# Performance work log

Measured on AMD Instinct MI355X. Metric: run time of the kernel, lower is better.

Reference implementation:

```python
import jax, jax.numpy as jnp
import numpy as np

GROUP_SIZE = 128
IN_FEATURES = 8192
OUT_FEATURES = 28672
TOKENS = 32


def _dequantize(qweight, qzeros, scales):
    """ExLlama q4 dequant.
    qweight: (K//8, N) int32, 8 int4 values per word packed along k.
    qzeros:  (G, N//8) int32, 8 int4 zeros per word packed along n.
    scales:  (G, N) fp16.  g = k // GROUP_SIZE; w = s * (q - (z + 1)).
    """
    shifts = jnp.arange(8, dtype=jnp.int32) * 4
    K = qweight.shape[0] * 8
    N = qweight.shape[1]
    G = qzeros.shape[0]
    # unpack weights along k: (K//8, 8, N) -> (K, N)
    q = (qweight[:, None, :] >> shifts[None, :, None]) & 15
    q = q.reshape(K, N)
    # unpack zeros along n: (G, N//8, 8) -> (G, N)
    z = (qzeros[:, :, None] >> shifts[None, None, :]) & 15
    z = z.reshape(G, N)
    # group-wise dequant: reshape k into (G, GROUP_SIZE)
    qg = q.reshape(G, GROUP_SIZE, N).astype(jnp.float16)
    zf = (z + 1).astype(jnp.float16)[:, None, :]          # ExLlama stores zero-1
    w = (qg - zf) * scales[:, None, :]                    # (G, GS, N) fp16
    return w.reshape(K, N)


def setup_inputs() -> dict:
    key = jax.random.key(0)
    k1, k2, k3, k4, k5 = jax.random.split(key, 5)
    x = jax.random.normal(k1, (TOKENS, IN_FEATURES), dtype=jnp.float16)
    qweight = jax.random.randint(k2, (IN_FEATURES // 8, OUT_FEATURES),
                                 minval=-(2**31), maxval=2**31 - 1, dtype=jnp.int32)
    qzeros = jax.random.randint(k3, (IN_FEATURES // GROUP_SIZE, OUT_FEATURES // 8),
                                minval=-(2**31), maxval=2**31 - 1, dtype=jnp.int32)
    scales = (jax.random.uniform(k4, (IN_FEATURES // GROUP_SIZE, OUT_FEATURES),
                                 dtype=jnp.float32) * 0.01 + 0.001).astype(jnp.float16)
    bias = jax.random.normal(k5, (OUT_FEATURES,), dtype=jnp.float16)
    return {"x": x, "qweight": qweight, "qzeros": qzeros,
            "scales": scales, "bias": bias}


def reference(x, qweight, qzeros, scales, bias):
    w = _dequantize(qweight, qzeros, scales)              # (K, N) fp16
    out = jnp.matmul(x.astype(jnp.float16), w)            # (T, N)
    return out + bias
```

## Files before the change

kernel.cpp:

```cpp
#include <hip/hip_runtime.h>

#define T_TOK   32
#define KDIM    8192
#define NDIM    28672
#define NZW     3584
#define PHK     256
#define NPH     (KDIM / PHK)
#define GPP     (PHK / 128)
#define XROW    (PHK + 8)
#define XIT     ((T_TOK * PHK) / (256 * 8))

typedef _Float16 half8  __attribute__((ext_vector_type(8)));
typedef _Float16 half2v __attribute__((ext_vector_type(2)));
typedef float    f32x4  __attribute__((ext_vector_type(4)));
typedef unsigned uint4v __attribute__((ext_vector_type(4)));

__global__ __launch_bounds__(256)
void exllama_gemm_fullk(const int*   __restrict__ qweight,
                        const int*   __restrict__ qzeros,
                        const float* __restrict__ scales,
                        const float* __restrict__ x,
                        const float* __restrict__ bias,
                        float*       __restrict__ out)
{
    __shared__ alignas(16) _Float16 xs[2][T_TOK * XROW];

    const int tid  = threadIdx.x;
    const int lane = tid & 63;
    const int wav  = tid >> 6;
    const int quad = lane >> 4;
    const int l16  = lane & 15;
    const int n    = blockIdx.x * 64 + wav * 16 + l16;

    const float* xbase[XIT];
    int          lofs[XIT];
    #pragma unroll
    for (int it = 0; it < XIT; ++it) {
        const int e  = it * 2048 + tid * 8;
        const int t  = e >> 8;
        const int kl = e & (PHK - 1);
        xbase[it] = x + (size_t)t * KDIM + kl;
        lofs[it]  = t * XROW + kl;
    }

    f32x4 xlo[XIT], xhi[XIT];
    auto LOADX = [&](int p) {
        #pragma unroll
        for (int it = 0; it < XIT; ++it) {
            const float* xp = xbase[it] + p * PHK;
            xlo[it] = *(const f32x4*)xp;
            xhi[it] = *(const f32x4*)(xp + 4);
        }
    };
    auto CVTW = [&](_Float16* buf) {
        #pragma unroll
        for (int it = 0; it < XIT; ++it) {
            uint4v u;
            #pragma unroll
            for (int j = 0; j < 4; ++j)
                u[j] = __builtin_bit_cast(unsigned,
                          __builtin_amdgcn_cvt_pkrtz(xlo[it][j], xhi[it][j]));
            *(uint4v*)(buf + lofs[it]) = u;
        }
    };
    auto LOADQ = [&](unsigned* qw, half2v* sp, half2v* cp, int p) {
        #pragma unroll
        for (int g = 0; g < GPP; ++g) {
            const size_t rb = (size_t)(p * (PHK / 8) + g * 16 + quad) * NDIM + n;
            #pragma unroll
            for (int c = 0; c < 4; ++c)
                qw[g * 4 + c] = (unsigned)qweight[rb + (size_t)(c * 4) * NDIM];
            const float s  = scales[(size_t)(p * GPP + g) * NDIM + n];
            const int   zw = qzeros[(size_t)(p * GPP + g) * NZW + (n >> 3)];
            const int   z  = (zw >> ((n & 7) * 4)) & 15;
            const _Float16 sh = (_Float16)s;
            const _Float16 ch = (_Float16)(float)(-(1025 + z));
            sp[g] = (half2v){sh, sh};
            cp[g] = (half2v){ch, ch};
        }
    };

    f32x4 acc0 = (f32x4){0.f, 0.f, 0.f, 0.f};
    f32x4 acc1 = (f32x4){0.f, 0.f, 0.f, 0.f};
    auto COMPUTE = [&](const unsigned* qw, const half2v* sp, const half2v* cp,
                       const _Float16* buf) {
        #pragma unroll
        for (int g = 0; g < GPP; ++g) {
            #pragma unroll
            for (int c = 0; c < 4; ++c) {
                const int kloc = g * 128 + c * 32 + quad * 8;
                half8 a0 = *(const half8*)(buf + l16 * XROW + kloc);
                half8 a1 = *(const half8*)(buf + (l16 + 16) * XROW + kloc);
                const unsigned w = qw[g * 4 + c];
                uint4v bu;
                #pragma unroll
                for (int i = 0; i < 4; ++i) {
                    unsigned t = ((w >> (4 * i)) & 0x000F000Fu) | 0x64006400u;
                    half2v th = __builtin_bit_cast(half2v, t);
                    half2v r  = (th + cp[g]) * sp[g];
                    bu[i] = __builtin_bit_cast(unsigned, r);
                }
                half8 bf = __builtin_bit_cast(half8, bu);
                acc0 = __builtin_amdgcn_mfma_f32_16x16x32_f16(a0, bf, acc0, 0, 0, 0);
                acc1 = __builtin_amdgcn_mfma_f32_16x16x32_f16(a1, bf, acc1, 0, 0, 0);
            }
        }
    };

    unsigned qwA[4 * GPP], qwB[4 * GPP];
    half2v   spA[GPP], cpA[GPP], spB[GPP], cpB[GPP];

    LOADX(0);
    LOADQ(qwA, spA, cpA, 0);
    CVTW(xs[0]);
    __syncthreads();

    for (int pp = 0; pp < NPH; pp += 2) {
        LOADX(pp + 1);
        LOADQ(qwB, spB, cpB, pp + 1);
        COMPUTE(qwA, spA, cpA, xs[0]);
        CVTW(xs[1]);
        __syncthreads();
        if (pp + 2 < NPH) {
            LOADX(pp + 2);
            LOADQ(qwA, spA, cpA, pp + 2);
        }
        COMPUTE(qwB, spB, cpB, xs[1]);
        if (pp + 2 < NPH) CVTW(xs[0]);
        __syncthreads();
    }

    const float bb = bias[n];
    #pragma unroll
    for (int r = 0; r < 4; ++r) {
        out[(size_t)(quad * 4 + r) * NDIM + n]        = acc0[r] + bb;
        out[(size_t)(16 + quad * 4 + r) * NDIM + n]   = acc1[r] + bb;
    }
}

extern "C" void kernel_launch(void* const* d_in, const int* in_sizes, int n_in,
                              void* d_out, int out_size, void* d_ws, size_t ws_size,
                              hipStream_t stream)
{
    const float* x  = (const float*)d_in[0];
    const int* qweight = (const int*)d_in[1];
    const int* qzeros  = (const int*)d_in[2];
    const float* sc = (const float*)d_in[3];
    const float* bs = (const float*)d_in[4];
    float* out      = (float*)d_out;

    (void)d_ws; (void)ws_size;
    exllama_gemm_fullk<<<dim3(NDIM / 64), 256, 0, stream>>>(
        qweight, qzeros, sc, x, bs, out);
}
```

Baseline: 211.0 us.

## Split K across blocks with workspace partials and separate reduce-bias kernel

```diff
diff --git a/kernel.cpp b/kernel.cpp
--- a/kernel.cpp
+++ b/kernel.cpp
@@ -5,24 +5,29 @@
 #define NDIM    28672
 #define NZW     3584
 #define PHK     256
-#define NPH     (KDIM / PHK)
 #define GPP     (PHK / 128)
 #define XROW    (PHK + 8)
 #define XIT     ((T_TOK * PHK) / (256 * 8))
+#define KSPLIT  4
 
 typedef _Float16 half8  __attribute__((ext_vector_type(8)));
 typedef _Float16 half2v __attribute__((ext_vector_type(2)));
 typedef float    f32x4  __attribute__((ext_vector_type(4)));
 typedef unsigned uint4v __attribute__((ext_vector_type(4)));
 
+template<int SPLIT>
 __global__ __launch_bounds__(256)
-void exllama_gemm_fullk(const int*   __restrict__ qweight,
-                        const int*   __restrict__ qzeros,
-                        const float* __restrict__ scales,
-                        const float* __restrict__ x,
-                        const float* __restrict__ bias,
-                        float*       __restrict__ out)
+void exllama_gemm(const int*   __restrict__ qweight,
+                  const int*   __restrict__ qzeros,
+                  const float* __restrict__ scales,
+                  const float* __restrict__ x,
+                  const float* __restrict__ bias,
+                  float*       __restrict__ ws,
+                  float*       __restrict__ out)
 {
+    constexpr int KSEG = KDIM / SPLIT;
+    constexpr int NPH  = KSEG / PHK;
+
     __shared__ alignas(16) _Float16 xs[2][T_TOK * XROW];
 
     const int tid  = threadIdx.x;
@@ -31,6 +36,8 @@
     const int quad = lane >> 4;
     const int l16  = lane & 15;
     const int n    = blockIdx.x * 64 + wav * 16 + l16;
+    const int seg  = (SPLIT > 1) ? blockIdx.y : 0;
+    const int k0   = seg * KSEG;
 
     const float* xbase[XIT];
     int          lofs[XIT];
@@ -39,7 +46,7 @@
         const int e  = it * 2048 + tid * 8;
         const int t  = e >> 8;
         const int kl = e & (PHK - 1);
-        xbase[it] = x + (size_t)t * KDIM + kl;
+        xbase[it] = x + (size_t)t * KDIM + k0 + kl;
         lofs[it]  = t * XROW + kl;
     }
 
@@ -66,12 +73,14 @@
     auto LOADQ = [&](unsigned* qw, half2v* sp, half2v* cp, int p) {
         #pragma unroll
         for (int g = 0; g < GPP; ++g) {
-            const size_t rb = (size_t)(p * (PHK / 8) + g * 16 + quad) * NDIM + n;
+            const int prow = (k0 >> 3) + p * (PHK / 8);
+            const size_t rb = (size_t)(prow + g * 16 + quad) * NDIM + n;
             #pragma unroll
             for (int c = 0; c < 4; ++c)
                 qw[g * 4 + c] = (unsigned)qweight[rb + (size_t)(c * 4) * NDIM];
-            const float s  = scales[(size_t)(p * GPP + g) * NDIM + n];
-            const int   zw = qzeros[(size_t)(p * GPP + g) * NZW + (n >> 3)];
+            const int gi = (k0 >> 7) + p * GPP + g;
+            const float s  = scales[(size_t)gi * NDIM + n];
+            const int   zw = qzeros[(size_t)gi * NZW + (n >> 3)];
             const int   z  = (zw >> ((n & 7) * 4)) & 15;
             const _Float16 sh = (_Float16)s;
             const _Float16 ch = (_Float16)(float)(-(1025 + z));
@@ -130,12 +139,36 @@
         __syncthreads();
     }
 
-    const float bb = bias[n];
+    if (SPLIT == 1) {
+        const float bb = bias[n];
+        #pragma unroll
+        for (int r = 0; r < 4; ++r) {
+            out[(size_t)(quad * 4 + r) * NDIM + n]      = acc0[r] + bb;
+            out[(size_t)(16 + quad * 4 + r) * NDIM + n] = acc1[r] + bb;
+        }
+    } else {
+        float* wsp = ws + (size_t)seg * (T_TOK * NDIM);
+        #pragma unroll
+        for (int r = 0; r < 4; ++r) {
+            wsp[(size_t)(quad * 4 + r) * NDIM + n]      = acc0[r];
+            wsp[(size_t)(16 + quad * 4 + r) * NDIM + n] = acc1[r];
+        }
+    }
+}
+
+__global__ __launch_bounds__(256)
+void reduce_bias(const float* __restrict__ ws,
+                 const float* __restrict__ bias,
+                 float*       __restrict__ out)
+{
+    const int e = (blockIdx.x * 256 + threadIdx.x) * 4;
+    const int n = e % NDIM;
+    f32x4 sum = (f32x4){0.f, 0.f, 0.f, 0.f};
     #pragma unroll
-    for (int r = 0; r < 4; ++r) {
-        out[(size_t)(quad * 4 + r) * NDIM + n]        = acc0[r] + bb;
-        out[(size_t)(16 + quad * 4 + r) * NDIM + n]   = acc1[r] + bb;
-    }
+    for (int s = 0; s < KSPLIT; ++s)
+        sum += *(const f32x4*)(ws + (size_t)s * (T_TOK * NDIM) + e);
+    f32x4 bb = *(const f32x4*)(bias + n);
+    *(f32x4*)(out + e) = sum + bb;
 }
 
 extern "C" void kernel_launch(void* const* d_in, const int* in_sizes, int n_in,
@@ -149,7 +182,14 @@
     const float* bs = (const float*)d_in[4];
     float* out      = (float*)d_out;
 
-    (void)d_ws; (void)ws_size;
-    exllama_gemm_fullk<<<dim3(NDIM / 64), 256, 0, stream>>>(
-        qweight, qzeros, sc, x, bs, out);
+    const size_t need = (size_t)KSPLIT * T_TOK * NDIM * sizeof(float);
+    if (ws_size >= need) {
+        exllama_gemm<KSPLIT><<<dim3(NDIM / 64, KSPLIT), 256, 0, stream>>>(
+            qweight, qzeros, sc, x, bs, (float*)d_ws, out);
+        reduce_bias<<<(T_TOK * NDIM) / (256 * 4), 256, 0, stream>>>(
+            (const float*)d_ws, bs, out);
+    } else {
+        exllama_gemm<1><<<dim3(NDIM / 64), 256, 0, stream>>>(
+            qweight, qzeros, sc, x, bs, nullptr, out);
+    }
 }
```

Result: faster. 206.5 us (-2.1%).
